# Performance work log

Hardware: AMD Instinct MI355X
Metric: run time of the kernel (lower is better)

## Reference

```python
import jax, jax.numpy as jnp
import numpy as np

BATCH = 1024
H = 1024  # input_size == hidden_size (forced by h0 = z.repeat)
STEPS = 4


def _uniform(key, shape, bound):
    return jax.random.uniform(key, shape, jnp.float32, -bound, bound)


def setup_inputs() -> dict:
    key = jax.random.key(0)
    ks = jax.random.split(key, 12)
    bound = 1.0 / np.sqrt(H)  # PyTorch LSTM/Linear default init range
    return {
        "z": jax.random.normal(ks[0], (BATCH, H), jnp.float32),
        # LSTM layer 0 (gate order: i, f, g, o)
        "W_ih0": _uniform(ks[1], (4 * H, H), bound),
        "W_hh0": _uniform(ks[2], (4 * H, H), bound),
        "b_ih0": _uniform(ks[3], (4 * H,), bound),
        "b_hh0": _uniform(ks[4], (4 * H,), bound),
        # LSTM layer 1
        "W_ih1": _uniform(ks[5], (4 * H, H), bound),
        "W_hh1": _uniform(ks[6], (4 * H, H), bound),
        "b_ih1": _uniform(ks[7], (4 * H,), bound),
        "b_hh1": _uniform(ks[8], (4 * H,), bound),
        # Output linear
        "W_lin": _uniform(ks[9], (H, H), bound),
        "b_lin": _uniform(ks[10], (H,), bound),
    }


def _lstm_cell(x, h, c, W_ih, W_hh, b_ih, b_hh):
    # PyTorch LSTM cell: gates = x W_ih^T + h W_hh^T + b_ih + b_hh, order i,f,g,o
    gates = x @ W_ih.T + h @ W_hh.T + (b_ih + b_hh)
    i, f, g, o = jnp.split(gates, 4, axis=-1)
    c_new = jax.nn.sigmoid(f) * c + jax.nn.sigmoid(i) * jnp.tanh(g)
    h_new = jax.nn.sigmoid(o) * jnp.tanh(c_new)
    return h_new, c_new


def reference(z, W_ih0, W_hh0, b_ih0, b_hh0, W_ih1, W_hh1, b_ih1, b_hh1, W_lin, b_lin):
    # init_hidden: both layers' h and c start as z; input each step is the constant z
    def step(carry, _):
        h0, c0, h1, c1 = carry
        h0, c0 = _lstm_cell(z, h0, c0, W_ih0, W_hh0, b_ih0, b_hh0)
        h1, c1 = _lstm_cell(h0, h1, c1, W_ih1, W_hh1, b_ih1, b_hh1)
        return (h0, c0, h1, c1), h1

    init = (z, z, z, z)
    _, outs = jax.lax.scan(step, init, None, length=STEPS)  # [4, B, H]
    feat = jnp.transpose(outs, (1, 0, 2))  # [B, 4, H]
    return feat @ W_lin.T + b_lin
```

## Files before the change

### kernel.cpp

```cpp
#include <hip/hip_runtime.h>
#include <hip/hip_bf16.h>
#include <cstdint>
#include <cstddef>


typedef __bf16 bf16_t;
typedef __bf16 bf16x8 __attribute__((ext_vector_type(8)));
typedef __bf16 bf16x4 __attribute__((ext_vector_type(4)));
typedef float f32x4 __attribute__((ext_vector_type(4)));

__device__ __forceinline__ void gload_lds16(const bf16_t* g, bf16_t* l) {
    __builtin_amdgcn_global_load_lds(
        (const __attribute__((address_space(1))) void*)g,
        (__attribute__((address_space(3))) void*)l,
        16, 0, 0);
}

__device__ __forceinline__ float sigmoid_f(float x) {
    return 1.f / (1.f + __expf(-x));
}
__device__ __forceinline__ float tanh_fast(float x) {
    const float t = __expf(2.f * x);
    return 1.f - 2.f / (t + 1.f);
}

__device__ __forceinline__ void gemm_core(
    const bf16_t* __restrict__ A, int lda,
    const bf16_t* __restrict__ B, int ldb,
    int K, int brow, int bcol,
    bf16_t* lsA, bf16_t* lsB, f32x4 acc[4][2])
{
    const int tid  = threadIdx.x;
    const int lane = tid & 63;
    const int wave = tid >> 6;
    const int wm = (wave >> 2) * 64;
    const int wn = (wave & 3) * 32;
    const int srow = lane >> 3;
    const int ssw  = ((lane & 7) ^ srow) * 8;
    const int ch0  = wave * 2;
    const int nkt  = K >> 6;

    auto stage = [&](int buf, int ktel) {
#pragma unroll
        for (int it = 0; it < 2; ++it) {
            const int ch = ch0 + it;
            const int row = ch * 8 + srow;
            gload_lds16(A + (size_t)(brow + row) * lda + ktel + ssw, &lsA[buf * 8192 + ch * 512]);
            gload_lds16(B + (size_t)(bcol + row) * ldb + ktel + ssw, &lsB[buf * 8192 + ch * 512]);
        }
    };

    stage(0, 0);
    __syncthreads();

    const int fr  = lane & 15;
    const int g8  = (lane >> 4) * 8;
    const int rsw = (fr & 7) * 8;

    for (int kt = 0; kt < nkt; ++kt) {
        const int buf = kt & 1;
        if (kt + 1 < nkt) stage(buf ^ 1, (kt + 1) << 6);
#pragma unroll
        for (int kk = 0; kk < 2; ++kk) {
            const int ko = (kk * 32 + g8) ^ rsw;
            bf16x8 af[4], bfv[2];
#pragma unroll
            for (int m = 0; m < 4; ++m)
                af[m] = *(const bf16x8*)&lsA[buf * 8192 + (wm + m * 16 + fr) * 64 + ko];
#pragma unroll
            for (int n = 0; n < 2; ++n)
                bfv[n] = *(const bf16x8*)&lsB[buf * 8192 + (wn + n * 16 + fr) * 64 + ko];
#pragma unroll
            for (int m = 0; m < 4; ++m)
#pragma unroll
                for (int n = 0; n < 2; ++n)
                    acc[m][n] = __builtin_amdgcn_mfma_f32_16x16x32_bf16(af[m], bfv[n], acc[m][n], 0, 0, 0);
        }
        __syncthreads();
    }
}

struct Job {
    const bf16_t* A;
    const bf16_t* B;
    const float*  add;
    const float*  bias;
    float*        c;
    bf16_t*       h1;
    bf16_t*       h2;
    float*        C;
    int lda, K, h1s, h2s, mode;
};

__global__ __launch_bounds__(512, 4) void fused_multi(Job j0, Job j1, Job j2, int n0, int n01)
{
    __shared__ __align__(16) float gsm[16384];

    const int bid = blockIdx.x;
    Job ja; int local, n;
    if (bid < n0)        { ja = j0; local = bid;       n = n0; }
    else if (bid < n01)  { ja = j1; local = bid - n0;  n = n01 - n0; }
    else                 { ja = j2; local = bid - n01; n = (int)gridDim.x - n01; }

    const int q    = n >> 3;
    const int tile = (local & 7) * q + (local >> 3);
    const int bcol = (tile >> 3) * 128;
    const int brow = (tile & 7) * 128;

    f32x4 acc[4][2] = {};
    bf16_t* ls = (bf16_t*)gsm;
    gemm_core(ja.A, ja.lda, ja.B, ja.K, ja.K, brow, bcol, ls, ls + 16384, acc);

    const int tid  = threadIdx.x;
    const int lane = tid & 63;
    const int wave = tid >> 6;
    const int wm = (wave >> 2) * 64;
    const int wn = (wave & 3) * 32;
    const int cr = (lane >> 4) * 4;
    const int cc = lane & 15;

    if (ja.mode == 1) {
#pragma unroll
        for (int nn = 0; nn < 2; ++nn) {
            const int col = bcol + wn + nn * 16 + cc;
            const float bv = ja.bias ? ja.bias[col] : 0.f;
#pragma unroll
            for (int m = 0; m < 4; ++m) {
                const int row0 = brow + wm + m * 16 + cr;
#pragma unroll
                for (int r = 0; r < 4; ++r)
                    ja.C[(size_t)(row0 + r) * 4096 + col] = acc[m][nn][r] + bv;
            }
        }
        return;
    }

#pragma unroll
    for (int nn = 0; nn < 2; ++nn)
#pragma unroll
        for (int m = 0; m < 4; ++m)
#pragma unroll
            for (int r = 0; r < 4; ++r)
                gsm[(wm + m * 16 + cr + r) * 128 + wn + nn * 16 + cc] = acc[m][nn][r];
    __syncthreads();

#pragma unroll
    for (int p = 0; p < 8; ++p) {
        const int idx = p * 512 + tid;
        const int rl = idx >> 5;
        const int nn = idx & 31;
        float4 gv = *(const float4*)&gsm[rl * 128 + nn * 4];
        const int grow = brow + rl;
        const int j0c = bcol + nn * 4;
        if (ja.add) {
            const float4 av = *(const float4*)&ja.add[(size_t)grow * 4096 + j0c];
            gv.x += av.x; gv.y += av.y; gv.z += av.z; gv.w += av.w;
        }
        if (ja.bias) {
            const float4 bv = *(const float4*)&ja.bias[j0c];
            gv.x += bv.x; gv.y += bv.y; gv.z += bv.z; gv.w += bv.w;
        }
        const int ng = j0c >> 2;
        const size_t ci = (size_t)grow * 1024 + ng;
        const float cn = sigmoid_f(gv.y) * ja.c[ci] + sigmoid_f(gv.x) * tanh_fast(gv.z);
        const float h  = sigmoid_f(gv.w) * tanh_fast(cn);
        ja.c[ci] = cn;
        const bf16_t hb = (bf16_t)h;
        ja.h1[(size_t)grow * ja.h1s + ng] = hb;
        if (ja.h2) ja.h2[(size_t)grow * ja.h2s + ng] = hb;
    }
}

__global__ __launch_bounds__(256) void prep_all(
    const float* __restrict__ z,
    const float4* __restrict__ Wih0, const float4* __restrict__ Whh0,
    const float4* __restrict__ Wih1, const float4* __restrict__ Whh1,
    const float4* __restrict__ Wlin,
    const float* __restrict__ bih0, const float* __restrict__ bhh0,
    const float* __restrict__ bih1, const float* __restrict__ bhh1,
    bf16x4* __restrict__ Wih0R, bf16x4* __restrict__ Whh0R, bf16x4* __restrict__ Wsum0R,
    bf16x4* __restrict__ WcatR1, bf16x4* __restrict__ Wlinb,
    bf16_t* __restrict__ zb, bf16_t* __restrict__ X0,
    float* __restrict__ c0, float* __restrict__ c1,
    float* __restrict__ b0R, float* __restrict__ b1R)
{
    const int t = blockIdx.x * 256 + threadIdx.x;
    if (t < 1048576) {
        const int j = t >> 8, col = t & 255;
        const int g = j & 3, nn = j >> 2;
        const int src = (g * 1024 + nn) * 256 + col;
        const float4 a = Wih0[src];
        const float4 b = Whh0[src];
        bf16x4 va = {(bf16_t)a.x, (bf16_t)a.y, (bf16_t)a.z, (bf16_t)a.w};
        bf16x4 vb = {(bf16_t)b.x, (bf16_t)b.y, (bf16_t)b.z, (bf16_t)b.w};
        bf16x4 vs = {(bf16_t)(a.x + b.x), (bf16_t)(a.y + b.y),
                     (bf16_t)(a.z + b.z), (bf16_t)(a.w + b.w)};
        Wih0R[t] = va; Whh0R[t] = vb; Wsum0R[t] = vs;
    } else if (t < 2097152) {
        const int i = t - 1048576;
        const int j = i >> 8, col = i & 255;
        const int g = j & 3, nn = j >> 2;
        const int src = (g * 1024 + nn) * 256 + col;
        const float4 a = Wih1[src];
        const float4 b = Whh1[src];
        bf16x4 va = {(bf16_t)a.x, (bf16_t)a.y, (bf16_t)a.z, (bf16_t)a.w};
        bf16x4 vb = {(bf16_t)b.x, (bf16_t)b.y, (bf16_t)b.z, (bf16_t)b.w};
        WcatR1[j * 512 + col]       = va;
        WcatR1[j * 512 + 256 + col] = vb;
    } else if (t < 2359296) {
        const int i = t - 2097152;
        const float4 a = Wlin[i];
        bf16x4 v = {(bf16_t)a.x, (bf16_t)a.y, (bf16_t)a.z, (bf16_t)a.w};
        Wlinb[i] = v;
    } else if (t < 2621440) {
        const int i = t - 2359296;
        const int b = i >> 8, n4 = i & 255;
        const float4 v = ((const float4*)z)[i];
        bf16x4 hv = {(bf16_t)v.x, (bf16_t)v.y, (bf16_t)v.z, (bf16_t)v.w};
        ((bf16x4*)zb)[i] = hv;
        *(bf16x4*)(X0 + (size_t)b * 2048 + 1024 + n4 * 4) = hv;
        ((float4*)c0)[i] = v;
        ((float4*)c1)[i] = v;
    } else if (t < 2622464) {
        const int nn = t - 2621440;
        float4 b0, b1;
        float* p0 = (float*)&b0; float* p1 = (float*)&b1;
#pragma unroll
        for (int g = 0; g < 4; ++g) {
            p0[g] = bih0[g * 1024 + nn] + bhh0[g * 1024 + nn];
            p1[g] = bih1[g * 1024 + nn] + bhh1[g * 1024 + nn];
        }
        ((float4*)b0R)[nn] = b0;
        ((float4*)b1R)[nn] = b1;
    }
}

extern "C" void kernel_launch(void* const* d_in, const int* in_sizes, int n_in,
                              void* d_out, int out_size, void* d_ws, size_t ws_size,
                              hipStream_t stream)
{
    const float* z     = (const float*)d_in[0];
    const float* W_ih0 = (const float*)d_in[1];
    const float* W_hh0 = (const float*)d_in[2];
    const float* b_ih0 = (const float*)d_in[3];
    const float* b_hh0 = (const float*)d_in[4];
    const float* W_ih1 = (const float*)d_in[5];
    const float* W_hh1 = (const float*)d_in[6];
    const float* b_ih1 = (const float*)d_in[7];
    const float* b_hh1 = (const float*)d_in[8];
    const float* W_lin = (const float*)d_in[9];
    const float* b_lin = (const float*)d_in[10];
    float* out = (float*)d_out;

    char* ws = (char*)d_ws;
    const size_t MB = 1u << 20;
    bf16_t* WcatR1 = (bf16_t*)(ws);
    bf16_t* Whh0R  = (bf16_t*)(ws + 16 * MB);
    bf16_t* Wih0R  = (bf16_t*)(ws + 24 * MB);
    bf16_t* Wsum0R = (bf16_t*)(ws + 32 * MB);
    bf16_t* Wlinb  = (bf16_t*)(ws + 40 * MB);
    bf16_t* zb     = (bf16_t*)(ws + 42 * MB);
    bf16_t* Xbuf   = (bf16_t*)(ws + 44 * MB);
    float*  Gz0R   = (float*) (ws + 52 * MB);
    bf16_t* stash  = (bf16_t*)(ws + 68 * MB);
    float*  c0     = (float*) (ws + 76 * MB);
    float*  c1     = (float*) (ws + 80 * MB);
    float*  bias0R = (float*) (ws + 84 * MB);
    float*  bias1R = (float*) (ws + 84 * MB + 16384);
    bf16_t* X[2] = {Xbuf, Xbuf + (size_t)(1u << 21)};

    prep_all<<<10244, 256, 0, stream>>>(
        z, (const float4*)W_ih0, (const float4*)W_hh0,
        (const float4*)W_ih1, (const float4*)W_hh1, (const float4*)W_lin,
        b_ih0, b_hh0, b_ih1, b_hh1,
        (bf16x4*)Wih0R, (bf16x4*)Whh0R, (bf16x4*)Wsum0R,
        (bf16x4*)WcatR1, (bf16x4*)Wlinb,
        zb, X[0], c0, c1, bias0R, bias1R);

    Job empty = {};

    {
        Job gz = {};
        gz.A = zb; gz.lda = 1024; gz.B = Wih0R; gz.K = 1024;
        gz.bias = bias0R; gz.C = Gz0R; gz.mode = 1;
        Job f00 = {};
        f00.A = zb; f00.lda = 1024; f00.B = Wsum0R; f00.K = 1024;
        f00.bias = bias0R; f00.c = c0; f00.h1 = X[0]; f00.h1s = 2048; f00.mode = 0;
        fused_multi<<<512, 512, 0, stream>>>(gz, f00, empty, 256, 512);
    }

    for (int t = 0; t < 4; ++t) {
        const int p = t & 1;
        Job a0 = {};
        a0.A = X[p]; a0.lda = 2048; a0.B = WcatR1; a0.K = 2048;
        a0.bias = bias1R; a0.c = c1;
        a0.h1 = stash + (size_t)t * (1u << 20); a0.h1s = 1024;
        if (t < 3) { a0.h2 = X[p ^ 1] + 1024; a0.h2s = 2048; }
        a0.mode = 0;

        Job a1 = {};
        if (t < 3) {
            a1.A = X[p]; a1.lda = 2048; a1.B = Whh0R; a1.K = 1024;
            a1.add = Gz0R; a1.c = c0; a1.h1 = X[p ^ 1]; a1.h1s = 2048; a1.mode = 0;
        }

        Job lj = {};
        if (t >= 1) {
            lj.A = stash + (size_t)(t - 1) * (1u << 20); lj.lda = 1024;
            lj.B = Wlinb; lj.K = 1024; lj.bias = b_lin;
            lj.C = out + (size_t)(t - 1) * 1024; lj.mode = 1;
        }

        if (t == 0)      fused_multi<<<512, 512, 0, stream>>>(a0, a1, empty, 256, 512);
        else if (t < 3)  fused_multi<<<576, 512, 0, stream>>>(a0, a1, lj, 256, 512);
        else             fused_multi<<<320, 512, 0, stream>>>(a0, lj, empty, 256, 320);
    }

    {
        Job lj = {};
        lj.A = stash + (size_t)3 * (1u << 20); lj.lda = 1024;
        lj.B = Wlinb; lj.K = 1024; lj.bias = b_lin;
        lj.C = out + (size_t)3 * 1024; lj.mode = 1;
        fused_multi<<<64, 512, 0, stream>>>(lj, empty, empty, 64, 64);
    }
}
```

Baseline: 220.1 us.

## Use 256-thread blocks with 64x64 warp tiles and single-buffered LDS

The GEMM tile is reorganised from 8 waves with 64x32 warp tiles into 4 waves with 64x64 warp tiles, so each wave issues more MFMAs per LDS fragment load. The LDS double buffer is dropped in favour of a single 32KB buffer with load/sync/compute/sync per k-step, and the LSTM epilogue is split into two 64-column halves so it fits the smaller shared buffer. This trades the overlap of global loads with compute for higher register-level reuse and lower LDS use per block, and it relies on more blocks per CU to hide load latency.

Result: slower. 247.0 us (+12.2%).

```diff
diff --git a/kernel.cpp b/kernel.cpp
--- a/kernel.cpp
+++ b/kernel.cpp
@@ -22,62 +22,6 @@
 __device__ __forceinline__ float tanh_fast(float x) {
     const float t = __expf(2.f * x);
     return 1.f - 2.f / (t + 1.f);
-}
-
-__device__ __forceinline__ void gemm_core(
-    const bf16_t* __restrict__ A, int lda,
-    const bf16_t* __restrict__ B, int ldb,
-    int K, int brow, int bcol,
-    bf16_t* lsA, bf16_t* lsB, f32x4 acc[4][2])
-{
-    const int tid  = threadIdx.x;
-    const int lane = tid & 63;
-    const int wave = tid >> 6;
-    const int wm = (wave >> 2) * 64;
-    const int wn = (wave & 3) * 32;
-    const int srow = lane >> 3;
-    const int ssw  = ((lane & 7) ^ srow) * 8;
-    const int ch0  = wave * 2;
-    const int nkt  = K >> 6;
-
-    auto stage = [&](int buf, int ktel) {
-#pragma unroll
-        for (int it = 0; it < 2; ++it) {
-            const int ch = ch0 + it;
-            const int row = ch * 8 + srow;
-            gload_lds16(A + (size_t)(brow + row) * lda + ktel + ssw, &lsA[buf * 8192 + ch * 512]);
-            gload_lds16(B + (size_t)(bcol + row) * ldb + ktel + ssw, &lsB[buf * 8192 + ch * 512]);
-        }
-    };
-
-    stage(0, 0);
-    __syncthreads();
-
-    const int fr  = lane & 15;
-    const int g8  = (lane >> 4) * 8;
-    const int rsw = (fr & 7) * 8;
-
-    for (int kt = 0; kt < nkt; ++kt) {
-        const int buf = kt & 1;
-        if (kt + 1 < nkt) stage(buf ^ 1, (kt + 1) << 6);
-#pragma unroll
-        for (int kk = 0; kk < 2; ++kk) {
-            const int ko = (kk * 32 + g8) ^ rsw;
-            bf16x8 af[4], bfv[2];
-#pragma unroll
-            for (int m = 0; m < 4; ++m)
-                af[m] = *(const bf16x8*)&lsA[buf * 8192 + (wm + m * 16 + fr) * 64 + ko];
-#pragma unroll
-            for (int n = 0; n < 2; ++n)
-                bfv[n] = *(const bf16x8*)&lsB[buf * 8192 + (wn + n * 16 + fr) * 64 + ko];
-#pragma unroll
-            for (int m = 0; m < 4; ++m)
-#pragma unroll
-                for (int n = 0; n < 2; ++n)
-                    acc[m][n] = __builtin_amdgcn_mfma_f32_16x16x32_bf16(af[m], bfv[n], acc[m][n], 0, 0, 0);
-        }
-        __syncthreads();
-    }
 }
 
 struct Job {
@@ -92,9 +36,12 @@
     int lda, K, h1s, h2s, mode;
 };
 
-__global__ __launch_bounds__(512, 4) void fused_multi(Job j0, Job j1, Job j2, int n0, int n01)
+__global__ __launch_bounds__(256, 3) void fused_multi(Job j0, Job j1, Job j2, int n0, int n01)
 {
-    __shared__ __align__(16) float gsm[16384];
+    __shared__ __align__(16) char smem[32768];
+    bf16_t* lsA = (bf16_t*)smem;
+    bf16_t* lsB = (bf16_t*)(smem + 16384);
+    float*  gsm = (float*)smem;
 
     const int bid = blockIdx.x;
     Job ja; int local, n;
@@ -107,21 +54,58 @@
     const int bcol = (tile >> 3) * 128;
     const int brow = (tile & 7) * 128;
 
-    f32x4 acc[4][2] = {};
-    bf16_t* ls = (bf16_t*)gsm;
-    gemm_core(ja.A, ja.lda, ja.B, ja.K, ja.K, brow, bcol, ls, ls + 16384, acc);
-
     const int tid  = threadIdx.x;
     const int lane = tid & 63;
     const int wave = tid >> 6;
-    const int wm = (wave >> 2) * 64;
-    const int wn = (wave & 3) * 32;
+    const int wm = (wave >> 1) * 64;
+    const int wn = (wave & 1) * 64;
+
+    const int srow = lane >> 3;
+    const int ssw  = ((lane & 7) ^ srow) * 8;
+    const int ch0  = wave * 4;
+    const int nkt  = ja.K >> 6;
+
+    const int fr  = lane & 15;
+    const int g8  = (lane >> 4) * 8;
+    const int rsw = (fr & 7) * 8;
+
+    f32x4 acc[4][4] = {};
+
+    for (int kt = 0; kt < nkt; ++kt) {
+        const int ktel = kt << 6;
+#pragma unroll
+        for (int it = 0; it < 4; ++it) {
+            const int ch = ch0 + it;
+            const int row = ch * 8 + srow;
+            gload_lds16(ja.A + (size_t)(brow + row) * ja.lda + ktel + ssw, &lsA[ch * 512]);
+            gload_lds16(ja.B + (size_t)(bcol + row) * ja.K   + ktel + ssw, &lsB[ch * 512]);
+        }
+        __syncthreads();
+#pragma unroll
+        for (int kk = 0; kk < 2; ++kk) {
+            const int ko = (kk * 32 + g8) ^ rsw;
+            bf16x8 af[4], bfv[4];
+#pragma unroll
+            for (int m = 0; m < 4; ++m)
+                af[m] = *(const bf16x8*)&lsA[(wm + m * 16 + fr) * 64 + ko];
+#pragma unroll
+            for (int nn = 0; nn < 4; ++nn)
+                bfv[nn] = *(const bf16x8*)&lsB[(wn + nn * 16 + fr) * 64 + ko];
+#pragma unroll
+            for (int m = 0; m < 4; ++m)
+#pragma unroll
+                for (int nn = 0; nn < 4; ++nn)
+                    acc[m][nn] = __builtin_amdgcn_mfma_f32_16x16x32_bf16(af[m], bfv[nn], acc[m][nn], 0, 0, 0);
+        }
+        __syncthreads();
+    }
+
     const int cr = (lane >> 4) * 4;
     const int cc = lane & 15;
 
     if (ja.mode == 1) {
 #pragma unroll
-        for (int nn = 0; nn < 2; ++nn) {
+        for (int nn = 0; nn < 4; ++nn) {
             const int col = bcol + wn + nn * 16 + cc;
             const float bv = ja.bias ? ja.bias[col] : 0.f;
 #pragma unroll
@@ -136,38 +120,43 @@
     }
 
 #pragma unroll
-    for (int nn = 0; nn < 2; ++nn)
-#pragma unroll
-        for (int m = 0; m < 4; ++m)
-#pragma unroll
-            for (int r = 0; r < 4; ++r)
-                gsm[(wm + m * 16 + cr + r) * 128 + wn + nn * 16 + cc] = acc[m][nn][r];
-    __syncthreads();
-
-#pragma unroll
-    for (int p = 0; p < 8; ++p) {
-        const int idx = p * 512 + tid;
-        const int rl = idx >> 5;
-        const int nn = idx & 31;
-        float4 gv = *(const float4*)&gsm[rl * 128 + nn * 4];
-        const int grow = brow + rl;
-        const int j0c = bcol + nn * 4;
-        if (ja.add) {
-            const float4 av = *(const float4*)&ja.add[(size_t)grow * 4096 + j0c];
-            gv.x += av.x; gv.y += av.y; gv.z += av.z; gv.w += av.w;
-        }
-        if (ja.bias) {
-            const float4 bv = *(const float4*)&ja.bias[j0c];
-            gv.x += bv.x; gv.y += bv.y; gv.z += bv.z; gv.w += bv.w;
-        }
-        const int ng = j0c >> 2;
-        const size_t ci = (size_t)grow * 1024 + ng;
-        const float cn = sigmoid_f(gv.y) * ja.c[ci] + sigmoid_f(gv.x) * tanh_fast(gv.z);
-        const float h  = sigmoid_f(gv.w) * tanh_fast(cn);
-        ja.c[ci] = cn;
-        const bf16_t hb = (bf16_t)h;
-        ja.h1[(size_t)grow * ja.h1s + ng] = hb;
-        if (ja.h2) ja.h2[(size_t)grow * ja.h2s + ng] = hb;
+    for (int h = 0; h < 2; ++h) {
+        if ((wave & 1) == h) {
+#pragma unroll
+            for (int nn = 0; nn < 4; ++nn)
+#pragma unroll
+                for (int m = 0; m < 4; ++m)
+#pragma unroll
+                    for (int r = 0; r < 4; ++r)
+                        gsm[(wm + m * 16 + cr + r) * 64 + nn * 16 + cc] = acc[m][nn][r];
+        }
+        __syncthreads();
+#pragma unroll
+        for (int p = 0; p < 8; ++p) {
+            const int idx = p * 256 + tid;
+            const int rl = idx >> 4;
+            const int nn = idx & 15;
+            float4 gv = *(const float4*)&gsm[rl * 64 + nn * 4];
+            const int grow = brow + rl;
+            const int j0c = bcol + h * 64 + nn * 4;
+            if (ja.add) {
+                const float4 av = *(const float4*)&ja.add[(size_t)grow * 4096 + j0c];
+                gv.x += av.x; gv.y += av.y; gv.z += av.z; gv.w += av.w;
+            }
+            if (ja.bias) {
+                const float4 bv = *(const float4*)&ja.bias[j0c];
+                gv.x += bv.x; gv.y += bv.y; gv.z += bv.z; gv.w += bv.w;
+            }
+            const int ng = j0c >> 2;
+            const size_t ci = (size_t)grow * 1024 + ng;
+            const float cn = sigmoid_f(gv.y) * ja.c[ci] + sigmoid_f(gv.x) * tanh_fast(gv.z);
+            const float hh = sigmoid_f(gv.w) * tanh_fast(cn);
+            ja.c[ci] = cn;
+            const bf16_t hb = (bf16_t)hh;
+            ja.h1[(size_t)grow * ja.h1s + ng] = hb;
+            if (ja.h2) ja.h2[(size_t)grow * ja.h2s + ng] = hb;
+        }
+        __syncthreads();
     }
 }
 
@@ -286,7 +275,7 @@
         Job f00 = {};
         f00.A = zb; f00.lda = 1024; f00.B = Wsum0R; f00.K = 1024;
         f00.bias = bias0R; f00.c = c0; f00.h1 = X[0]; f00.h1s = 2048; f00.mode = 0;
-        fused_multi<<<512, 512, 0, stream>>>(gz, f00, empty, 256, 512);
+        fused_multi<<<512, 256, 0, stream>>>(gz, f00, empty, 256, 512);
     }
 
     for (int t = 0; t < 4; ++t) {
@@ -311,9 +300,9 @@
             lj.C = out + (size_t)(t - 1) * 1024; lj.mode = 1;
         }
 
-        if (t == 0)      fused_multi<<<512, 512, 0, stream>>>(a0, a1, empty, 256, 512);
-        else if (t < 3)  fused_multi<<<576, 512, 0, stream>>>(a0, a1, lj, 256, 512);
-        else             fused_multi<<<320, 512, 0, stream>>>(a0, lj, empty, 256, 320);
+        if (t == 0)      fused_multi<<<512, 256, 0, stream>>>(a0, a1, empty, 256, 512);
+        else if (t < 3)  fused_multi<<<576, 256, 0, stream>>>(a0, a1, lj, 256, 512);
+        else             fused_multi<<<320, 256, 0, stream>>>(a0, lj, empty, 256, 320);
     }
 
     {
@@ -321,6 +310,6 @@
         lj.A = stash + (size_t)3 * (1u << 20); lj.lda = 1024;
         lj.B = Wlinb; lj.K = 1024; lj.bias = b_lin;
         lj.C = out + (size_t)3 * 1024; lj.mode = 1;
-        fused_multi<<<64, 512, 0, stream>>>(lj, empty, empty, 64, 64);
-    }
-}
+        fused_multi<<<64, 256, 0, stream>>>(lj, empty, empty, 64, 64);
+    }
+}
```

## Restructure GEMM pipeline with split-wait barriers, swizzled epilogue, and hoisted layer-1 z-term

Applied to the files above, without the earlier changes.

The GEMM main loop now uses a 64KB double buffer and waits with explicit s_waitcnt vmcnt plus raw s_barrier, which should let the next tile's loads overlap the current MFMAs and drops one barrier per iteration. The epilogue LDS staging uses an XOR swizzle to reduce bank conflicts. The layer-1 step-0 product of the z input (h1 initial = z) with W_hh1 is precomputed in the first launch alongside the other z-GEMMs, so step 0 of layer 1 runs with K=1024 instead of 2048. The costs are a larger first launch and more LDS per block, which may lower occupancy.

After: 215.2 us. 2.2% less time.

```diff
diff --git a/kernel.cpp b/kernel.cpp
--- a/kernel.cpp
+++ b/kernel.cpp
@@ -22,62 +22,6 @@
 __device__ __forceinline__ float tanh_fast(float x) {
     const float t = __expf(2.f * x);
     return 1.f - 2.f / (t + 1.f);
-}
-
-__device__ __forceinline__ void gemm_core(
-    const bf16_t* __restrict__ A, int lda,
-    const bf16_t* __restrict__ B, int ldb,
-    int K, int brow, int bcol,
-    bf16_t* lsA, bf16_t* lsB, f32x4 acc[4][2])
-{
-    const int tid  = threadIdx.x;
-    const int lane = tid & 63;
-    const int wave = tid >> 6;
-    const int wm = (wave >> 2) * 64;
-    const int wn = (wave & 3) * 32;
-    const int srow = lane >> 3;
-    const int ssw  = ((lane & 7) ^ srow) * 8;
-    const int ch0  = wave * 2;
-    const int nkt  = K >> 6;
-
-    auto stage = [&](int buf, int ktel) {
-#pragma unroll
-        for (int it = 0; it < 2; ++it) {
-            const int ch = ch0 + it;
-            const int row = ch * 8 + srow;
-            gload_lds16(A + (size_t)(brow + row) * lda + ktel + ssw, &lsA[buf * 8192 + ch * 512]);
-            gload_lds16(B + (size_t)(bcol + row) * ldb + ktel + ssw, &lsB[buf * 8192 + ch * 512]);
-        }
-    };
-
-    stage(0, 0);
-    __syncthreads();
-
-    const int fr  = lane & 15;
-    const int g8  = (lane >> 4) * 8;
-    const int rsw = (fr & 7) * 8;
-
-    for (int kt = 0; kt < nkt; ++kt) {
-        const int buf = kt & 1;
-        if (kt + 1 < nkt) stage(buf ^ 1, (kt + 1) << 6);
-#pragma unroll
-        for (int kk = 0; kk < 2; ++kk) {
-            const int ko = (kk * 32 + g8) ^ rsw;
-            bf16x8 af[4], bfv[2];
-#pragma unroll
-            for (int m = 0; m < 4; ++m)
-                af[m] = *(const bf16x8*)&lsA[buf * 8192 + (wm + m * 16 + fr) * 64 + ko];
-#pragma unroll
-            for (int n = 0; n < 2; ++n)
-                bfv[n] = *(const bf16x8*)&lsB[buf * 8192 + (wn + n * 16 + fr) * 64 + ko];
-#pragma unroll
-            for (int m = 0; m < 4; ++m)
-#pragma unroll
-                for (int n = 0; n < 2; ++n)
-                    acc[m][n] = __builtin_amdgcn_mfma_f32_16x16x32_bf16(af[m], bfv[n], acc[m][n], 0, 0, 0);
-        }
-        __syncthreads();
-    }
 }
 
 struct Job {
@@ -89,12 +33,13 @@
     bf16_t*       h1;
     bf16_t*       h2;
     float*        C;
-    int lda, K, h1s, h2s, mode;
+    int lda, ldb, K, h1s, h2s, mode;
 };
 
 __global__ __launch_bounds__(512, 4) void fused_multi(Job j0, Job j1, Job j2, int n0, int n01)
 {
-    __shared__ __align__(16) float gsm[16384];
+    __shared__ __align__(16) char smem[65536];
+    float* gsm = (float*)smem;
 
     const int bid = blockIdx.x;
     Job ja; int local, n;
@@ -107,15 +52,71 @@
     const int bcol = (tile >> 3) * 128;
     const int brow = (tile & 7) * 128;
 
-    f32x4 acc[4][2] = {};
-    bf16_t* ls = (bf16_t*)gsm;
-    gemm_core(ja.A, ja.lda, ja.B, ja.K, ja.K, brow, bcol, ls, ls + 16384, acc);
-
     const int tid  = threadIdx.x;
     const int lane = tid & 63;
     const int wave = tid >> 6;
     const int wm = (wave >> 2) * 64;
     const int wn = (wave & 3) * 32;
+
+    const int srow = lane >> 3;
+    const int ssw  = ((lane & 7) ^ srow) * 8;
+    const int ch0  = wave * 2;
+    const int nkt  = ja.K >> 6;
+
+    const int fr  = lane & 15;
+    const int g8  = (lane >> 4) * 8;
+    const int rsw = (fr & 7) * 8;
+
+    f32x4 acc[4][2] = {};
+
+    auto stage = [&](int buf, int ktel) {
+        bf16_t* lsA = (bf16_t*)(smem + buf * 32768);
+        bf16_t* lsB = (bf16_t*)(smem + buf * 32768 + 16384);
+#pragma unroll
+        for (int it = 0; it < 2; ++it) {
+            const int ch = ch0 + it;
+            const int row = ch * 8 + srow;
+            gload_lds16(ja.A + (size_t)(brow + row) * ja.lda + ktel + ssw, &lsA[ch * 512]);
+            gload_lds16(ja.B + (size_t)(bcol + row) * ja.ldb + ktel + ssw, &lsB[ch * 512]);
+        }
+    };
+
+    stage(0, 0);
+
+    for (int kt = 0; kt < nkt; ++kt) {
+        const int buf = kt & 1;
+        if (kt + 1 < nkt) {
+            stage(buf ^ 1, (kt + 1) << 6);
+            asm volatile("s_waitcnt vmcnt(4)" ::: "memory");
+        } else {
+            asm volatile("s_waitcnt vmcnt(0)" ::: "memory");
+        }
+        __builtin_amdgcn_sched_barrier(0);
+        __builtin_amdgcn_s_barrier();
+        __builtin_amdgcn_sched_barrier(0);
+
+        const bf16_t* lsA = (const bf16_t*)(smem + buf * 32768);
+        const bf16_t* lsB = (const bf16_t*)(smem + buf * 32768 + 16384);
+#pragma unroll
+        for (int kk = 0; kk < 2; ++kk) {
+            const int ko = (kk * 32 + g8) ^ rsw;
+            bf16x8 af[4], bfv[2];
+#pragma unroll
+            for (int m = 0; m < 4; ++m)
+                af[m] = *(const bf16x8*)&lsA[(wm + m * 16 + fr) * 64 + ko];
+#pragma unroll
+            for (int nn = 0; nn < 2; ++nn)
+                bfv[nn] = *(const bf16x8*)&lsB[(wn + nn * 16 + fr) * 64 + ko];
+#pragma unroll
+            for (int m = 0; m < 4; ++m)
+#pragma unroll
+                for (int nn = 0; nn < 2; ++nn)
+                    acc[m][nn] = __builtin_amdgcn_mfma_f32_16x16x32_bf16(af[m], bfv[nn], acc[m][nn], 0, 0, 0);
+        }
+        __builtin_amdgcn_sched_barrier(0);
+        __builtin_amdgcn_s_barrier();
+    }
+
     const int cr = (lane >> 4) * 4;
     const int cc = lane & 15;
 
@@ -140,8 +141,11 @@
 #pragma unroll
         for (int m = 0; m < 4; ++m)
 #pragma unroll
-            for (int r = 0; r < 4; ++r)
-                gsm[(wm + m * 16 + cr + r) * 128 + wn + nn * 16 + cc] = acc[m][nn][r];
+            for (int r = 0; r < 4; ++r) {
+                const int row = wm + m * 16 + cr + r;
+                const int col = wn + nn * 16 + cc;
+                gsm[row * 128 + (col ^ (((row >> 2) & 1) << 4))] = acc[m][nn][r];
+            }
     __syncthreads();
 
 #pragma unroll
@@ -149,7 +153,7 @@
         const int idx = p * 512 + tid;
         const int rl = idx >> 5;
         const int nn = idx & 31;
-        float4 gv = *(const float4*)&gsm[rl * 128 + nn * 4];
+        float4 gv = *(const float4*)&gsm[rl * 128 + ((nn * 4) ^ (((rl >> 2) & 1) << 4))];
         const int grow = brow + rl;
         const int j0c = bcol + nn * 4;
         if (ja.add) {
@@ -163,9 +167,9 @@
         const int ng = j0c >> 2;
         const size_t ci = (size_t)grow * 1024 + ng;
         const float cn = sigmoid_f(gv.y) * ja.c[ci] + sigmoid_f(gv.x) * tanh_fast(gv.z);
-        const float h  = sigmoid_f(gv.w) * tanh_fast(cn);
+        const float hh = sigmoid_f(gv.w) * tanh_fast(cn);
         ja.c[ci] = cn;
-        const bf16_t hb = (bf16_t)h;
+        const bf16_t hb = (bf16_t)hh;
         ja.h1[(size_t)grow * ja.h1s + ng] = hb;
         if (ja.h2) ja.h2[(size_t)grow * ja.h2s + ng] = hb;
     }
@@ -267,6 +271,7 @@
     float*  c1     = (float*) (ws + 80 * MB);
     float*  bias0R = (float*) (ws + 84 * MB);
     float*  bias1R = (float*) (ws + 84 * MB + 16384);
+    float*  Gz1R   = (float*) (ws + 88 * MB);
     bf16_t* X[2] = {Xbuf, Xbuf + (size_t)(1u << 21)};
 
     prep_all<<<10244, 256, 0, stream>>>(
@@ -281,33 +286,42 @@
 
     {
         Job gz = {};
-        gz.A = zb; gz.lda = 1024; gz.B = Wih0R; gz.K = 1024;
+        gz.A = zb; gz.lda = 1024; gz.B = Wih0R; gz.ldb = 1024; gz.K = 1024;
         gz.bias = bias0R; gz.C = Gz0R; gz.mode = 1;
         Job f00 = {};
-        f00.A = zb; f00.lda = 1024; f00.B = Wsum0R; f00.K = 1024;
+        f00.A = zb; f00.lda = 1024; f00.B = Wsum0R; f00.ldb = 1024; f00.K = 1024;
         f00.bias = bias0R; f00.c = c0; f00.h1 = X[0]; f00.h1s = 2048; f00.mode = 0;
-        fused_multi<<<512, 512, 0, stream>>>(gz, f00, empty, 256, 512);
+        Job gz1 = {};
+        gz1.A = zb; gz1.lda = 1024; gz1.B = WcatR1 + 1024; gz1.ldb = 2048; gz1.K = 1024;
+        gz1.bias = bias1R; gz1.C = Gz1R; gz1.mode = 1;
+        fused_multi<<<768, 512, 0, stream>>>(gz, f00, gz1, 256, 512);
     }
 
     for (int t = 0; t < 4; ++t) {
         const int p = t & 1;
         Job a0 = {};
-        a0.A = X[p]; a0.lda = 2048; a0.B = WcatR1; a0.K = 2048;
-        a0.bias = bias1R; a0.c = c1;
+        if (t == 0) {
+            a0.A = X[0]; a0.lda = 2048; a0.B = WcatR1; a0.ldb = 2048; a0.K = 1024;
+            a0.add = Gz1R; a0.bias = nullptr;
+        } else {
+            a0.A = X[p]; a0.lda = 2048; a0.B = WcatR1; a0.ldb = 2048; a0.K = 2048;
+            a0.bias = bias1R;
+        }
+        a0.c = c1;
         a0.h1 = stash + (size_t)t * (1u << 20); a0.h1s = 1024;
         if (t < 3) { a0.h2 = X[p ^ 1] + 1024; a0.h2s = 2048; }
         a0.mode = 0;
 
         Job a1 = {};
         if (t < 3) {
-            a1.A = X[p]; a1.lda = 2048; a1.B = Whh0R; a1.K = 1024;
+            a1.A = X[p]; a1.lda = 2048; a1.B = Whh0R; a1.ldb = 1024; a1.K = 1024;
             a1.add = Gz0R; a1.c = c0; a1.h1 = X[p ^ 1]; a1.h1s = 2048; a1.mode = 0;
         }
 
         Job lj = {};
         if (t >= 1) {
             lj.A = stash + (size_t)(t - 1) * (1u << 20); lj.lda = 1024;
-            lj.B = Wlinb; lj.K = 1024; lj.bias = b_lin;
+            lj.B = Wlinb; lj.ldb = 1024; lj.K = 1024; lj.bias = b_lin;
             lj.C = out + (size_t)(t - 1) * 1024; lj.mode = 1;
         }
 
@@ -319,7 +333,7 @@
     {
         Job lj = {};
         lj.A = stash + (size_t)3 * (1u << 20); lj.lda = 1024;
-        lj.B = Wlinb; lj.K = 1024; lj.bias = b_lin;
+        lj.B = Wlinb; lj.ldb = 1024; lj.K = 1024; lj.bias = b_lin;
         lj.C = out + (size_t)3 * 1024; lj.mode = 1;
         fused_multi<<<64, 512, 0, stream>>>(lj, empty, empty, 64, 64);
     }
```
